# Performance work log

Hardware: AMD Instinct MI355X
Metric: run time of the kernel (lower is better)

Reference implementation:

```python
import jax, jax.numpy as jnp
import numpy as np

N = 50000      # nodes
E = 800000     # edges (before self loops)
IN = 128       # input_dim
ED = 16        # edge_dim
HID = 32       # hidden_dim (per-head out_channels)
H = 4          # heads
OUT = 64       # output_dim
NEG = 0.1      # negative_slope
EPS = 1e-5     # batchnorm eps


def setup_inputs() -> dict:
    key = jax.random.key(0)
    ks = jax.random.split(key, 32)
    s = 0.1
    p = {}
    p["x"] = jax.random.normal(ks[0], (N, IN), jnp.float32)
    p["edge_index"] = jax.random.randint(ks[1], (2, E), 0, N, dtype=jnp.int32)
    p["edge_attr"] = jax.random.normal(ks[2], (E, ED), jnp.float32)
    # input embed: Linear(IN, HID) + BatchNorm1d (eval-mode running stats)
    p["W0"] = jax.random.normal(ks[3], (HID, IN), jnp.float32) * s
    p["b0"] = jnp.zeros((HID,), jnp.float32)
    p["bn_g"] = jnp.ones((HID,), jnp.float32)
    p["bn_b"] = jnp.zeros((HID,), jnp.float32)
    p["bn_m"] = jnp.zeros((HID,), jnp.float32)
    p["bn_v"] = jnp.ones((HID,), jnp.float32)
    # two GATv2Conv layers: lin_l, lin_r [H*HID, HID] (+bias), lin_edge [H*HID, ED] (no bias),
    # att [H, HID], out bias [HID] (concat=False)
    k = 4
    for l in range(2):
        p[f"Wl{l}"] = jax.random.normal(ks[k + 0], (H * HID, HID), jnp.float32) * s
        p[f"bl{l}"] = jnp.zeros((H * HID,), jnp.float32)
        p[f"Wr{l}"] = jax.random.normal(ks[k + 1], (H * HID, HID), jnp.float32) * s
        p[f"br{l}"] = jnp.zeros((H * HID,), jnp.float32)
        p[f"We{l}"] = jax.random.normal(ks[k + 2], (H * HID, ED), jnp.float32) * s
        p[f"att{l}"] = jax.random.normal(ks[k + 3], (H, HID), jnp.float32) * s
        p[f"bias{l}"] = jnp.zeros((HID,), jnp.float32)
        k += 4
    p["Wout"] = jax.random.normal(ks[k], (OUT, HID), jnp.float32) * s
    p["bout"] = jnp.zeros((OUT,), jnp.float32)
    return p


def _gatv2(x, src, dst, eattr, Wl, bl, Wr, br, We, att, bias):
    # x: [N, HID]; src/dst: [Et]; eattr: [Et, ED]
    xl = (x @ Wl.T + bl).reshape(N, H, HID)   # source transform
    xr = (x @ Wr.T + br).reshape(N, H, HID)   # target transform
    ea = (eattr @ We.T).reshape(-1, H, HID)   # edge transform
    m = jax.nn.leaky_relu(xl[src] + xr[dst] + ea, NEG)   # [Et, H, HID]
    alpha = jnp.einsum('ehc,hc->eh', m, att)             # [Et, H]
    amax = jax.ops.segment_max(alpha, dst, num_segments=N)  # every node has a self loop
    ex = jnp.exp(alpha - amax[dst])
    den = jax.ops.segment_sum(ex, dst, num_segments=N)
    w = ex / den[dst]                                    # segment softmax [Et, H]
    out = jax.ops.segment_sum(xl[src] * w[:, :, None], dst, num_segments=N)  # [N, H, HID]
    return out.mean(axis=1) + bias                       # concat=False -> mean heads


def reference(x, edge_index, edge_attr,
              W0, b0, bn_g, bn_b, bn_m, bn_v,
              Wl0, bl0, Wr0, br0, We0, att0, bias0,
              Wl1, bl1, Wr1, br1, We1, att1, bias1,
              Wout, bout):
    src, dst = edge_index[0], edge_index[1]
    # input embed: Linear + BatchNorm1d(eval) + LeakyReLU(0.1)
    e = x @ W0.T + b0
    e = (e - bn_m) / jnp.sqrt(bn_v + EPS) * bn_g + bn_b
    e = jax.nn.leaky_relu(e, NEG)
    # add self loops once (same both layers): fill_value='mean' => per-dst mean edge_attr
    cnt = jax.ops.segment_sum(jnp.ones((E,), jnp.float32), dst, num_segments=N)
    loop_attr = jax.ops.segment_sum(edge_attr, dst, num_segments=N) / jnp.maximum(cnt, 1.0)[:, None]
    ar = jnp.arange(N, dtype=src.dtype)
    src_f = jnp.concatenate([src, ar])
    dst_f = jnp.concatenate([dst, ar])
    ea_f = jnp.concatenate([edge_attr, loop_attr], axis=0)
    h = _gatv2(e, src_f, dst_f, ea_f, Wl0, bl0, Wr0, br0, We0, att0, bias0)
    h = _gatv2(h, src_f, dst_f, ea_f, Wl1, bl1, Wr1, br1, We1, att1, bias1)
    return jax.nn.leaky_relu(h @ Wout.T + bout, NEG)
```

## Files before the change

### kernel.cpp

```cpp
#include <hip/hip_runtime.h>
#include <hip/hip_fp16.h>
#include <math.h>

#define NN   50000
#define EE   800000
#define IND  128
#define EDD  16
#define HIDD 32
#define NH   4
#define HC   128
#define OUTD 64
#define NEG  0.1f
#define BN_EPS 1e-5f
#define LOG2E 1.44269504088896340736f

typedef __attribute__((ext_vector_type(2))) float v2f;
typedef __attribute__((ext_vector_type(2))) _Float16 v2h;

#if defined(__has_builtin)
#  if __has_builtin(__builtin_amdgcn_fdot2)
#    define HAVE_FDOT2 1
#  else
#    define HAVE_FDOT2 0
#  endif
#else
#  define HAVE_FDOT2 0
#endif

__device__ __forceinline__ float lrelu(float x) { return fmaxf(x, NEG * x); }
__device__ __forceinline__ v2f lrelu2(v2f v) { return __builtin_elementwise_max(v, v * NEG); }
__device__ __forceinline__ float2 unpk(float f) {
    return __half22float2(__builtin_bit_cast(__half2, f));
}

#define DPPADD(p, CTRL) do {                                                     \
    int _t = __builtin_amdgcn_update_dpp(0, __builtin_bit_cast(int, (p)),        \
                                         (CTRL), 0xF, 0xF, true);                \
    (p) += __builtin_bit_cast(float, _t);                                        \
} while (0)

__global__ void count_fold_kernel(const int* __restrict__ ei, int* __restrict__ cnt,
                                  int* __restrict__ rank,
                                  const float* __restrict__ W0, const float* __restrict__ b0,
                                  const float* __restrict__ g, const float* __restrict__ bb,
                                  const float* __restrict__ bm, const float* __restrict__ bv,
                                  const float* __restrict__ Wl0, const float* __restrict__ Wr0,
                                  const float* __restrict__ Wl1, const float* __restrict__ Wr1,
                                  const float* __restrict__ We0, const float* __restrict__ We1,
                                  float* __restrict__ w0t, float* __restrict__ b0f,
                                  float* __restrict__ wlt0, float* __restrict__ wrt0,
                                  float* __restrict__ wlt1, float* __restrict__ wrt1,
                                  __half2* __restrict__ weh0, __half2* __restrict__ weh1) {
    if (blockIdx.x < EE / 256) {
        int e = blockIdx.x * 256 + threadIdx.x;
        rank[e] = atomicAdd(&cnt[ei[EE + e]], 1);
        return;
    }
    int tid = threadIdx.x;
    for (int idx = tid; idx < IND * HIDD; idx += 256) {
        int k = idx >> 5, c = idx & 31;
        float s = g[c] * (1.0f / sqrtf(bv[c] + BN_EPS));
        w0t[idx] = W0[c * IND + k] * s;
    }
    if (tid < HIDD) {
        float s = g[tid] * (1.0f / sqrtf(bv[tid] + BN_EPS));
        b0f[tid] = (b0[tid] - bm[tid]) * s + bb[tid];
    }
    for (int idx = tid; idx < HIDD * HC; idx += 256) {
        int k = idx >> 7, c = idx & 127;
        wlt0[idx] = Wl0[c * HIDD + k];
        wrt0[idx] = Wr0[c * HIDD + k];
        wlt1[idx] = Wl1[c * HIDD + k];
        wrt1[idx] = Wr1[c * HIDD + k];
    }
    for (int idx = tid; idx < HC * 8; idx += 256) {
        int c = idx >> 3, k = idx & 7;
        weh0[idx] = __floats2half2_rn(We0[c * EDD + 2 * k], We0[c * EDD + 2 * k + 1]);
        weh1[idx] = __floats2half2_rn(We1[c * EDD + 2 * k], We1[c * EDD + 2 * k + 1]);
    }
}

__global__ void scan1_kernel(const int* cnt, int* pre, int* bsum) {
    int i = blockIdx.x * 1024 + threadIdx.x;
    int lane = threadIdx.x & 63, wid = threadIdx.x >> 6;
    __shared__ int wsum[16];
    int v = (i < NN) ? cnt[i] : 0;
    int s = v;
    #pragma unroll
    for (int off = 1; off < 64; off <<= 1) {
        int t = __shfl_up(s, off);
        if (lane >= off) s += t;
    }
    if (lane == 63) wsum[wid] = s;
    __syncthreads();
    if (wid == 0) {
        int ws = (lane < 16) ? wsum[lane] : 0;
        #pragma unroll
        for (int off = 1; off < 16; off <<= 1) {
            int t = __shfl_up(ws, off);
            if (lane >= off) ws += t;
        }
        if (lane < 16) wsum[lane] = ws;
    }
    __syncthreads();
    int woff = (wid > 0) ? wsum[wid - 1] : 0;
    if (i < NN) pre[i] = woff + s - v;
    if (threadIdx.x == 1023) bsum[blockIdx.x] = wsum[15];
}

__global__ void scan3_kernel(int* rowstart, const int* pre, const int* bsum, int nb) {
    __shared__ int boff_s;
    if (threadIdx.x < 64) {
        int lane = threadIdx.x;
        int v = (lane < nb) ? bsum[lane] : 0;
        int s = v;
        #pragma unroll
        for (int off = 1; off < 64; off <<= 1) {
            int t = __shfl_up(s, off);
            if (lane >= off) s += t;
        }
        if (lane == (int)blockIdx.x) boff_s = s - v;
    }
    __syncthreads();
    int i = blockIdx.x * 1024 + threadIdx.x;
    if (i < NN) rowstart[i] = pre[i] + boff_s;
    if (i == 0) rowstart[NN] = EE;
}

__global__ void scatter_kernel(const int* __restrict__ ei, const int* __restrict__ rowstart,
                               const int* __restrict__ rank, const float* __restrict__ eattr,
                               int* __restrict__ csr_src, __half2* __restrict__ ea16) {
    int e = blockIdx.x * blockDim.x + threadIdx.x;
    if (e >= EE) return;
    int d = ei[EE + e];
    int pos = rowstart[d] + rank[e];
    csr_src[pos] = ei[e];
    const float4* src = (const float4*)(eattr + ((size_t)e << 4));
    float4 q0 = src[0], q1 = src[1], q2 = src[2], q3 = src[3];
    __half2 h[8];
    h[0] = __floats2half2_rn(q0.x, q0.y); h[1] = __floats2half2_rn(q0.z, q0.w);
    h[2] = __floats2half2_rn(q1.x, q1.y); h[3] = __floats2half2_rn(q1.z, q1.w);
    h[4] = __floats2half2_rn(q2.x, q2.y); h[5] = __floats2half2_rn(q2.z, q2.w);
    h[6] = __floats2half2_rn(q3.x, q3.y); h[7] = __floats2half2_rn(q3.z, q3.w);
    float4* dst = (float4*)(ea16 + ((size_t)pos << 3));
    dst[0] = *(float4*)&h[0];
    dst[1] = *(float4*)&h[4];
}

__global__ void embed_lin_kernel(const float* __restrict__ x,
                                 const float* __restrict__ w0t, const float* __restrict__ b0f,
                                 const float* __restrict__ wlt, const float* __restrict__ bl,
                                 const float* __restrict__ wrt, const float* __restrict__ br,
                                 __half2* __restrict__ xl, float* __restrict__ xr) {
    int tid = threadIdx.x;
    int n0 = blockIdx.x * 8;
    __shared__ float sx[8 * IND];
    __shared__ float se[8][HIDD];
    *(float4*)(sx + tid * 4) = *(const float4*)(x + (size_t)n0 * IND + tid * 4);
    __syncthreads();
    {
        int r = tid >> 5, c = tid & 31;
        float acc = b0f[c];
        const float* xrow = sx + r * IND;
        #pragma unroll 8
        for (int k = 0; k < IND; k++) acc += xrow[k] * w0t[k * HIDD + c];
        se[r][c] = lrelu(acc);
    }
    __syncthreads();
    int mat = tid >> 7, grp = (tid >> 6) & 1, pr = tid & 63;
    int c0 = 2 * pr;
    const float* WT = mat ? wrt : wlt;
    const float* b  = mat ? br : bl;
    v2f bv2 = (v2f){b[c0], b[c0 + 1]};
    v2f a0 = bv2, a1 = bv2, a2 = bv2, a3 = bv2;
    int nb = grp * 4;
    #pragma unroll
    for (int k = 0; k < HIDD; k++) {
        v2f wk = *(const v2f*)(WT + k * HC + c0);
        a0 += wk * se[nb + 0][k]; a1 += wk * se[nb + 1][k];
        a2 += wk * se[nb + 2][k]; a3 += wk * se[nb + 3][k];
    }
    if (mat == 0) {
        xl[((unsigned)(n0 + nb + 0) << 6) + pr] = __floats2half2_rn(a0.x, a0.y);
        xl[((unsigned)(n0 + nb + 1) << 6) + pr] = __floats2half2_rn(a1.x, a1.y);
        xl[((unsigned)(n0 + nb + 2) << 6) + pr] = __floats2half2_rn(a2.x, a2.y);
        xl[((unsigned)(n0 + nb + 3) << 6) + pr] = __floats2half2_rn(a3.x, a3.y);
    } else {
        *(float2*)(xr + ((unsigned)(n0 + nb + 0) << 7) + c0) = make_float2(a0.x, a0.y);
        *(float2*)(xr + ((unsigned)(n0 + nb + 1) << 7) + c0) = make_float2(a1.x, a1.y);
        *(float2*)(xr + ((unsigned)(n0 + nb + 2) << 7) + c0) = make_float2(a2.x, a2.y);
        *(float2*)(xr + ((unsigned)(n0 + nb + 3) << 7) + c0) = make_float2(a3.x, a3.y);
    }
}

__global__ void lin_kernel(const float* __restrict__ f,
                           const float* __restrict__ wlt, const float* __restrict__ bl,
                           const float* __restrict__ wrt, const float* __restrict__ br,
                           __half2* __restrict__ xl, float* __restrict__ xr) {
    int tid = threadIdx.x;
    int n0 = blockIdx.x * 8;
    __shared__ float se[8][HIDD];
    se[tid >> 5][tid & 31] = f[((unsigned)(n0 + (tid >> 5)) << 5) + (tid & 31)];
    __syncthreads();
    int mat = tid >> 7, grp = (tid >> 6) & 1, pr = tid & 63;
    int c0 = 2 * pr;
    const float* WT = mat ? wrt : wlt;
    const float* b  = mat ? br : bl;
    v2f bv2 = (v2f){b[c0], b[c0 + 1]};
    v2f a0 = bv2, a1 = bv2, a2 = bv2, a3 = bv2;
    int nb = grp * 4;
    #pragma unroll
    for (int k = 0; k < HIDD; k++) {
        v2f wk = *(const v2f*)(WT + k * HC + c0);
        a0 += wk * se[nb + 0][k]; a1 += wk * se[nb + 1][k];
        a2 += wk * se[nb + 2][k]; a3 += wk * se[nb + 3][k];
    }
    if (mat == 0) {
        xl[((unsigned)(n0 + nb + 0) << 6) + pr] = __floats2half2_rn(a0.x, a0.y);
        xl[((unsigned)(n0 + nb + 1) << 6) + pr] = __floats2half2_rn(a1.x, a1.y);
        xl[((unsigned)(n0 + nb + 2) << 6) + pr] = __floats2half2_rn(a2.x, a2.y);
        xl[((unsigned)(n0 + nb + 3) << 6) + pr] = __floats2half2_rn(a3.x, a3.y);
    } else {
        *(float2*)(xr + ((unsigned)(n0 + nb + 0) << 7) + c0) = make_float2(a0.x, a0.y);
        *(float2*)(xr + ((unsigned)(n0 + nb + 1) << 7) + c0) = make_float2(a1.x, a1.y);
        *(float2*)(xr + ((unsigned)(n0 + nb + 2) << 7) + c0) = make_float2(a2.x, a2.y);
        *(float2*)(xr + ((unsigned)(n0 + nb + 3) << 7) + c0) = make_float2(a3.x, a3.y);
    }
}

template<bool OUTHEAD>
__global__ void gat_fused_kernel(const __half2* __restrict__ xl, const float* __restrict__ xr,
                                 const __half2* __restrict__ ea16,
                                 const float* __restrict__ We,
                                 const __half2* __restrict__ weh,
                                 const float* __restrict__ att,
                                 const int* __restrict__ rowstart, const int* __restrict__ csr_src,
                                 const float* __restrict__ bias,
                                 const float* __restrict__ Wout, const float* __restrict__ bout,
                                 float* __restrict__ out) {
    int n = (blockIdx.x * blockDim.x + threadIdx.x) >> 6;
    int lane = threadIdx.x & 63;
    if (n >= NN) return;
    n = __builtin_amdgcn_readfirstlane(n);
    int start = __builtin_amdgcn_readfirstlane(rowstart[n]);
    int end   = __builtin_amdgcn_readfirstlane(rowstart[n + 1]);
    int deg = end - start;
    int c0 = 2 * lane;

    __half2 xLh = xl[((unsigned)n << 6) + lane];
    v2f xrv = *(const v2f*)(xr + ((unsigned)n << 7) + c0);
    v2f attv = *(const v2f*)(att + c0) * LOG2E;

#if HAVE_FDOT2
    (void)We;
    v2h wh0[8], wh1[8];
    {
        const float4* pw = (const float4*)(weh + (size_t)c0 * 8);
        float4 q0 = pw[0], q1 = pw[1], q2 = pw[2], q3 = pw[3];
        float t[16];
        *(float4*)(t)      = q0; *(float4*)(t + 4)  = q1;
        *(float4*)(t + 8)  = q2; *(float4*)(t + 12) = q3;
        #pragma unroll
        for (int k = 0; k < 8; k++) {
            wh0[k] = __builtin_bit_cast(v2h, t[k]);
            wh1[k] = __builtin_bit_cast(v2h, t[8 + k]);
        }
    }
    auto proj = [&](float4 r0, float4 r1) -> v2f {
        float e[8];
        *(float4*)(e) = r0; *(float4*)(e + 4) = r1;
        float a0 = 0.f, a1 = 0.f;
        #pragma unroll
        for (int k = 0; k < 8; k++) {
            v2h ek = __builtin_bit_cast(v2h, e[k]);
            a0 = __builtin_amdgcn_fdot2(ek, wh0[k], a0, false);
            a1 = __builtin_amdgcn_fdot2(ek, wh1[k], a1, false);
        }
        return (v2f){a0, a1};
    };
#else
    (void)weh;
    v2f wv[16];
    {
        const float* ra = We + c0 * EDD;
        const float* rb = ra + EDD;
        float4 a0 = *(const float4*)(ra),     a1 = *(const float4*)(ra + 4);
        float4 a2 = *(const float4*)(ra + 8), a3 = *(const float4*)(ra + 12);
        float4 b0 = *(const float4*)(rb),     b1 = *(const float4*)(rb + 4);
        float4 b2 = *(const float4*)(rb + 8), b3 = *(const float4*)(rb + 12);
        wv[0]=(v2f){a0.x,b0.x}; wv[1]=(v2f){a0.y,b0.y}; wv[2]=(v2f){a0.z,b0.z}; wv[3]=(v2f){a0.w,b0.w};
        wv[4]=(v2f){a1.x,b1.x}; wv[5]=(v2f){a1.y,b1.y}; wv[6]=(v2f){a1.z,b1.z}; wv[7]=(v2f){a1.w,b1.w};
        wv[8]=(v2f){a2.x,b2.x}; wv[9]=(v2f){a2.y,b2.y}; wv[10]=(v2f){a2.z,b2.z}; wv[11]=(v2f){a2.w,b2.w};
        wv[12]=(v2f){a3.x,b3.x}; wv[13]=(v2f){a3.y,b3.y}; wv[14]=(v2f){a3.z,b3.z}; wv[15]=(v2f){a3.w,b3.w};
    }
    auto proj = [&](float4 r0, float4 r1) -> v2f {
        float2 t0 = unpk(r0.x), t1 = unpk(r0.y), t2 = unpk(r0.z), t3 = unpk(r0.w);
        float2 t4 = unpk(r1.x), t5 = unpk(r1.y), t6 = unpk(r1.z), t7 = unpk(r1.w);
        return wv[0]*t0.x  + wv[1]*t0.y  + wv[2]*t1.x  + wv[3]*t1.y
             + wv[4]*t2.x  + wv[5]*t2.y  + wv[6]*t3.x  + wv[7]*t3.y
             + wv[8]*t4.x  + wv[9]*t4.y  + wv[10]*t5.x + wv[11]*t5.y
             + wv[12]*t6.x + wv[13]*t6.y + wv[14]*t7.x + wv[15]*t7.y;
    };
#endif

    float lh = 0.f;
    v2f acc   = (v2f){0.f, 0.f};
    v2f easum = (v2f){0.f, 0.f};

    auto proc = [&](v2f xv, v2f ea) {
        easum += ea;
        v2f z  = xv + xrv + ea;
        v2f mm = lrelu2(z);
        v2f pp = mm * attv;
        float p = pp.x + pp.y;
        DPPADD(p, 0xB1);
        DPPADD(p, 0x4E);
        DPPADD(p, 0x124);
        DPPADD(p, 0x128);
        float w = exp2f(p);
        lh  += w;
        acc += xv * w;
    };

    #define GATHER(i0, S0, S1, S2, S3, X0, X1, X2, X3, E0, E1, E2, E3) do {           \
        __half2 xh0 = xl[((unsigned)(S0) << 6) + lane];                                \
        __half2 xh1 = xl[((unsigned)(S1) << 6) + lane];                                \
        __half2 xh2 = xl[((unsigned)(S2) << 6) + lane];                                \
        __half2 xh3 = xl[((unsigned)(S3) << 6) + lane];                                \
        const float4* ep = (const float4*)(ea16 + ((size_t)(unsigned)(i0) << 3));      \
        float4 r00 = ep[0], r01 = ep[1], r10 = ep[2], r11 = ep[3];                     \
        float4 r20 = ep[4], r21 = ep[5], r30 = ep[6], r31 = ep[7];                     \
        E0 = proj(r00, r01); E1 = proj(r10, r11);                                      \
        E2 = proj(r20, r21); E3 = proj(r30, r31);                                      \
        float2 xf;                                                                     \
        xf = __half22float2(xh0); X0 = (v2f){xf.x, xf.y};                              \
        xf = __half22float2(xh1); X1 = (v2f){xf.x, xf.y};                              \
        xf = __half22float2(xh2); X2 = (v2f){xf.x, xf.y};                              \
        xf = __half22float2(xh3); X3 = (v2f){xf.x, xf.y};                              \
    } while (0)

    int i = start;
    int nf = deg >> 2;
    if (nf > 0) {
        int v0 = csr_src[i],     v1 = csr_src[i + 1],
            v2 = csr_src[i + 2], v3 = csr_src[i + 3];
        int j4 = (i + 4 > EE - 4) ? (EE - 4) : (i + 4);
        int u0 = csr_src[j4],     u1 = csr_src[j4 + 1],
            u2 = csr_src[j4 + 2], u3 = csr_src[j4 + 3];
        int s0 = __builtin_amdgcn_readfirstlane(v0), s1 = __builtin_amdgcn_readfirstlane(v1);
        int s2 = __builtin_amdgcn_readfirstlane(v2), s3 = __builtin_amdgcn_readfirstlane(v3);
        v2f A0x, A1x, A2x, A3x, A0e, A1e, A2e, A3e;
        GATHER(i, s0, s1, s2, s3, A0x, A1x, A2x, A3x, A0e, A1e, A2e, A3e);
        for (int k = 1; k < nf; k++) {
            int jn = i + 4 * (k + 1);
            jn = (jn > EE - 4) ? (EE - 4) : jn;
            int w0 = csr_src[jn],     w1 = csr_src[jn + 1],
                w2 = csr_src[jn + 2], w3 = csr_src[jn + 3];
            int t0 = __builtin_amdgcn_readfirstlane(u0), t1 = __builtin_amdgcn_readfirstlane(u1);
            int t2 = __builtin_amdgcn_readfirstlane(u2), t3 = __builtin_amdgcn_readfirstlane(u3);
            v2f B0x, B1x, B2x, B3x, B0e, B1e, B2e, B3e;
            GATHER(i + 4 * k, t0, t1, t2, t3, B0x, B1x, B2x, B3x, B0e, B1e, B2e, B3e);
            proc(A0x, A0e); proc(A1x, A1e); proc(A2x, A2e); proc(A3x, A3e);
            A0x = B0x; A1x = B1x; A2x = B2x; A3x = B3x;
            A0e = B0e; A1e = B1e; A2e = B2e; A3e = B3e;
            u0 = w0; u1 = w1; u2 = w2; u3 = w3;
        }
        proc(A0x, A0e); proc(A1x, A1e); proc(A2x, A2e); proc(A3x, A3e);
        i += 4 * nf;
    }
    int rem = end - i;
    if (rem > 0) {
        v2f Tx[3], Te[3];
        int sA = __builtin_amdgcn_readfirstlane(csr_src[i]);
        int sB = (rem > 1) ? __builtin_amdgcn_readfirstlane(csr_src[i + 1]) : sA;
        int sC = (rem > 2) ? __builtin_amdgcn_readfirstlane(csr_src[i + 2]) : sA;
        __half2 xh0 = xl[((unsigned)sA << 6) + lane];
        __half2 xh1 = xl[((unsigned)sB << 6) + lane];
        __half2 xh2 = xl[((unsigned)sC << 6) + lane];
        const float4* ep = (const float4*)(ea16 + ((size_t)(unsigned)i << 3));
        int lim2 = (rem > 1) ? 2 : 0, lim4 = (rem > 2) ? 4 : 0;
        float4 r00 = ep[0], r01 = ep[1];
        float4 r10 = ep[lim2], r11 = ep[lim2 + 1];
        float4 r20 = ep[lim4], r21 = ep[lim4 + 1];
        float2 xf;
        xf = __half22float2(xh0); Tx[0] = (v2f){xf.x, xf.y};
        xf = __half22float2(xh1); Tx[1] = (v2f){xf.x, xf.y};
        xf = __half22float2(xh2); Tx[2] = (v2f){xf.x, xf.y};
        Te[0] = proj(r00, r01); Te[1] = proj(r10, r11); Te[2] = proj(r20, r21);
        proc(Tx[0], Te[0]);
        if (rem > 1) proc(Tx[1], Te[1]);
        if (rem > 2) proc(Tx[2], Te[2]);
    }

    {
        float invdeg = 1.0f / (float)(deg > 0 ? deg : 1);
        float2 xf = __half22float2(xLh);
        proc((v2f){xf.x, xf.y}, easum * invdeg);
    }

    float inv = 1.0f / lh;
    float acc0 = acc.x * inv, acc1 = acc.y * inv;
    acc0 += __shfl_xor(acc0, 16); acc0 += __shfl_xor(acc0, 32);
    acc1 += __shfl_xor(acc1, 16); acc1 += __shfl_xor(acc1, 32);

    if (!OUTHEAD) {
        if (lane < 16) {
            float2 o = make_float2(acc0 * 0.25f + bias[2 * lane],
                                   acc1 * 0.25f + bias[2 * lane + 1]);
            *(float2*)(out + ((unsigned)n << 5) + 2 * lane) = o;
        }
    } else {
        __shared__ float sh[4][HIDD];
        int w = threadIdx.x >> 6;
        if (lane < 16) {
            sh[w][2 * lane]     = acc0 * 0.25f + bias[2 * lane];
            sh[w][2 * lane + 1] = acc1 * 0.25f + bias[2 * lane + 1];
        }
        float a = bout[lane];
        const float* wr = Wout + lane * HIDD;
        #pragma unroll
        for (int k = 0; k < HIDD; k++) a += sh[w][k] * wr[k];
        out[((unsigned)n << 6) + lane] = lrelu(a);
    }
    #undef GATHER
}

extern "C" void kernel_launch(void* const* d_in, const int* in_sizes, int n_in,
                              void* d_out, int out_size, void* d_ws, size_t ws_size,
                              hipStream_t stream) {
    const float* x     = (const float*)d_in[0];
    const int*   ei    = (const int*)  d_in[1];
    const float* eattr = (const float*)d_in[2];
    const float* W0    = (const float*)d_in[3];
    const float* b0    = (const float*)d_in[4];
    const float* bn_g  = (const float*)d_in[5];
    const float* bn_b  = (const float*)d_in[6];
    const float* bn_m  = (const float*)d_in[7];
    const float* bn_v  = (const float*)d_in[8];
    const float* Wl[2]   = { (const float*)d_in[9],  (const float*)d_in[16] };
    const float* bl[2]   = { (const float*)d_in[10], (const float*)d_in[17] };
    const float* Wr[2]   = { (const float*)d_in[11], (const float*)d_in[18] };
    const float* br[2]   = { (const float*)d_in[12], (const float*)d_in[19] };
    const float* We[2]   = { (const float*)d_in[13], (const float*)d_in[20] };
    const float* att[2]  = { (const float*)d_in[14], (const float*)d_in[21] };
    const float* bias[2] = { (const float*)d_in[15], (const float*)d_in[22] };
    const float* Wout  = (const float*)d_in[23];
    const float* bout  = (const float*)d_in[24];
    float* out = (float*)d_out;

    const int NB = (NN + 1023) / 1024;
    char* p = (char*)d_ws;
    auto carve = [&](size_t bytes) { char* r = p; p += (bytes + 255) & ~(size_t)255; return r; };
    float*   h1       = (float*)  carve((size_t)NN * HIDD * 4);
    __half2* xl       = (__half2*)carve((size_t)NN * HC * 2);
    float*   xr       = (float*)  carve((size_t)NN * HC * 4);
    int*     cnt      = (int*)    carve((size_t)NN * 4);
    int*     rank     = (int*)    carve((size_t)EE * 4);
    int*     pre      = (int*)    carve((size_t)NN * 4);
    int*     bsum     = (int*)    carve((size_t)64 * 4);
    int*     rowstart = (int*)    carve((size_t)(NN + 1) * 4);
    int*     csr_src  = (int*)    carve((size_t)EE * 4);
    __half2* ea16     = (__half2*)carve((size_t)EE * EDD * 2);
    float*   w0t      = (float*)  carve((size_t)IND * HIDD * 4);
    float*   b0f      = (float*)  carve((size_t)HIDD * 4);
    float*   wlt0     = (float*)  carve((size_t)HIDD * HC * 4);
    float*   wrt0     = (float*)  carve((size_t)HIDD * HC * 4);
    float*   wlt1     = (float*)  carve((size_t)HIDD * HC * 4);
    float*   wrt1     = (float*)  carve((size_t)HIDD * HC * 4);
    __half2* weh0     = (__half2*)carve((size_t)HC * 8 * 4);
    __half2* weh1     = (__half2*)carve((size_t)HC * 8 * 4);

    hipMemsetAsync(cnt, 0, (size_t)NN * 4, stream);

    count_fold_kernel<<<EE / 256 + 1, 256, 0, stream>>>(
        ei, cnt, rank, W0, b0, bn_g, bn_b, bn_m, bn_v,
        Wl[0], Wr[0], Wl[1], Wr[1], We[0], We[1],
        w0t, b0f, wlt0, wrt0, wlt1, wrt1, weh0, weh1);
    scan1_kernel<<<NB, 1024, 0, stream>>>(cnt, pre, bsum);
    scan3_kernel<<<NB, 1024, 0, stream>>>(rowstart, pre, bsum, NB);
    scatter_kernel<<<(EE + 255) / 256, 256, 0, stream>>>(ei, rowstart, rank, eattr,
                                                         csr_src, ea16);

    embed_lin_kernel<<<NN / 8, 256, 0, stream>>>(x, w0t, b0f, wlt0, bl[0], wrt0, br[0], xl, xr);
    gat_fused_kernel<false><<<(NN * 64) / 256, 256, 0, stream>>>(
        xl, xr, ea16, We[0], weh0, att[0], rowstart, csr_src, bias[0], nullptr, nullptr, h1);

    lin_kernel<<<NN / 8, 256, 0, stream>>>(h1, wlt1, bl[1], wrt1, br[1], xl, xr);
    gat_fused_kernel<true><<<(NN * 64) / 256, 256, 0, stream>>>(
        xl, xr, ea16, We[1], weh1, att[1], rowstart, csr_src, bias[1], Wout, bout, out);
}
```

Before: 474.5 us.

## Process two destination nodes per wavefront with four channels per lane

The GAT aggregation kernel now assigns two nodes to each 64-lane wave, one per 32-lane half, and each lane handles four channels instead of two. Edge loops run to the larger of the two degrees, with predicated weights, and read from a padded CSR tail so the separate remainder path goes away. Source indices are loaded cooperatively and shuffled instead of read with scalar loads. The aim is to halve the number of waves and improve memory-level parallelism for low-degree nodes, at the cost of divergence between the two halves' degrees and more registers per lane.

```diff
diff --git a/kernel.cpp b/kernel.cpp
--- a/kernel.cpp
+++ b/kernel.cpp
@@ -15,6 +15,7 @@
 #define LOG2E 1.44269504088896340736f
 
 typedef __attribute__((ext_vector_type(2))) float v2f;
+typedef __attribute__((ext_vector_type(4))) float v4f;
 typedef __attribute__((ext_vector_type(2))) _Float16 v2h;
 
 #if defined(__has_builtin)
@@ -28,8 +29,10 @@
 #endif
 
 __device__ __forceinline__ float lrelu(float x) { return fmaxf(x, NEG * x); }
-__device__ __forceinline__ v2f lrelu2(v2f v) { return __builtin_elementwise_max(v, v * NEG); }
-__device__ __forceinline__ float2 unpk(float f) {
+__device__ __forceinline__ float2 unpk(unsigned u) {
+    return __half22float2(__builtin_bit_cast(__half2, u));
+}
+__device__ __forceinline__ float2 unpkf(float f) {
     return __half22float2(__builtin_bit_cast(__half2, f));
 }
 
@@ -132,6 +135,12 @@
                                int* __restrict__ csr_src, __half2* __restrict__ ea16) {
     int e = blockIdx.x * blockDim.x + threadIdx.x;
     if (e >= EE) return;
+    if (e < 8) {
+        csr_src[EE + e] = 0;
+        float4* pd = (float4*)(ea16 + ((size_t)(EE + e) << 3));
+        pd[0] = make_float4(0.f, 0.f, 0.f, 0.f);
+        pd[1] = make_float4(0.f, 0.f, 0.f, 0.f);
+    }
     int d = ei[EE + e];
     int pos = rowstart[d] + rank[e];
     csr_src[pos] = ei[e];
@@ -229,198 +238,185 @@
 }
 
 template<bool OUTHEAD>
-__global__ void gat_fused_kernel(const __half2* __restrict__ xl, const float* __restrict__ xr,
+__global__ __launch_bounds__(256) void gat_fused_kernel(
+                                 const __half2* __restrict__ xl, const float* __restrict__ xr,
                                  const __half2* __restrict__ ea16,
-                                 const float* __restrict__ We,
                                  const __half2* __restrict__ weh,
                                  const float* __restrict__ att,
                                  const int* __restrict__ rowstart, const int* __restrict__ csr_src,
                                  const float* __restrict__ bias,
                                  const float* __restrict__ Wout, const float* __restrict__ bout,
                                  float* __restrict__ out) {
-    int n = (blockIdx.x * blockDim.x + threadIdx.x) >> 6;
+    int w = __builtin_amdgcn_readfirstlane(blockIdx.x * 4 + (threadIdx.x >> 6));
     int lane = threadIdx.x & 63;
-    if (n >= NN) return;
-    n = __builtin_amdgcn_readfirstlane(n);
-    int start = __builtin_amdgcn_readfirstlane(rowstart[n]);
-    int end   = __builtin_amdgcn_readfirstlane(rowstart[n + 1]);
-    int deg = end - start;
-    int c0 = 2 * lane;
-
-    __half2 xLh = xl[((unsigned)n << 6) + lane];
-    v2f xrv = *(const v2f*)(xr + ((unsigned)n << 7) + c0);
-    v2f attv = *(const v2f*)(att + c0) * LOG2E;
+    int half = (lane >> 5) & 1, hl = lane & 31;
+    int nA = 2 * w;
+    int sA = __builtin_amdgcn_readfirstlane(rowstart[nA]);
+    int sM = __builtin_amdgcn_readfirstlane(rowstart[nA + 1]);
+    int sE = __builtin_amdgcn_readfirstlane(rowstart[nA + 2]);
+    int degA = sM - sA, degB = sE - sM;
+    int dmax = degA > degB ? degA : degB;
+    int n     = half ? (nA + 1) : nA;
+    int start = half ? sM : sA;
+    int deg   = half ? degB : degA;
+    int c4 = 4 * hl;
+
+    uint2 xLh = *(const uint2*)(xl + ((unsigned)n << 6) + 2 * hl);
+    v4f xrv = *(const v4f*)(xr + ((size_t)n << 7) + c4);
+    v4f attv = *(const v4f*)(att + c4) * LOG2E;
 
 #if HAVE_FDOT2
-    (void)We;
-    v2h wh0[8], wh1[8];
+    v2h wh0[8], wh1[8], wh2[8], wh3[8];
     {
-        const float4* pw = (const float4*)(weh + (size_t)c0 * 8);
-        float4 q0 = pw[0], q1 = pw[1], q2 = pw[2], q3 = pw[3];
-        float t[16];
-        *(float4*)(t)      = q0; *(float4*)(t + 4)  = q1;
-        *(float4*)(t + 8)  = q2; *(float4*)(t + 12) = q3;
+        const float4* pw = (const float4*)(weh + (size_t)c4 * 8);
+        float t[32];
+        #pragma unroll
+        for (int q = 0; q < 8; q++) *(float4*)(t + 4 * q) = pw[q];
         #pragma unroll
         for (int k = 0; k < 8; k++) {
             wh0[k] = __builtin_bit_cast(v2h, t[k]);
             wh1[k] = __builtin_bit_cast(v2h, t[8 + k]);
-        }
-    }
-    auto proj = [&](float4 r0, float4 r1) -> v2f {
+            wh2[k] = __builtin_bit_cast(v2h, t[16 + k]);
+            wh3[k] = __builtin_bit_cast(v2h, t[24 + k]);
+        }
+    }
+    auto proj = [&](float4 r0, float4 r1) -> v4f {
         float e[8];
         *(float4*)(e) = r0; *(float4*)(e + 4) = r1;
-        float a0 = 0.f, a1 = 0.f;
+        float a0 = 0.f, a1 = 0.f, a2 = 0.f, a3 = 0.f;
         #pragma unroll
         for (int k = 0; k < 8; k++) {
             v2h ek = __builtin_bit_cast(v2h, e[k]);
             a0 = __builtin_amdgcn_fdot2(ek, wh0[k], a0, false);
             a1 = __builtin_amdgcn_fdot2(ek, wh1[k], a1, false);
-        }
-        return (v2f){a0, a1};
+            a2 = __builtin_amdgcn_fdot2(ek, wh2[k], a2, false);
+            a3 = __builtin_amdgcn_fdot2(ek, wh3[k], a3, false);
+        }
+        return (v4f){a0, a1, a2, a3};
     };
 #else
-    (void)weh;
-    v2f wv[16];
+    float wf0[16], wf1[16], wf2[16], wf3[16];
     {
-        const float* ra = We + c0 * EDD;
-        const float* rb = ra + EDD;
-        float4 a0 = *(const float4*)(ra),     a1 = *(const float4*)(ra + 4);
-        float4 a2 = *(const float4*)(ra + 8), a3 = *(const float4*)(ra + 12);
-        float4 b0 = *(const float4*)(rb),     b1 = *(const float4*)(rb + 4);
-        float4 b2 = *(const float4*)(rb + 8), b3 = *(const float4*)(rb + 12);
-        wv[0]=(v2f){a0.x,b0.x}; wv[1]=(v2f){a0.y,b0.y}; wv[2]=(v2f){a0.z,b0.z}; wv[3]=(v2f){a0.w,b0.w};
-        wv[4]=(v2f){a1.x,b1.x}; wv[5]=(v2f){a1.y,b1.y}; wv[6]=(v2f){a1.z,b1.z}; wv[7]=(v2f){a1.w,b1.w};
-        wv[8]=(v2f){a2.x,b2.x}; wv[9]=(v2f){a2.y,b2.y}; wv[10]=(v2f){a2.z,b2.z}; wv[11]=(v2f){a2.w,b2.w};
-        wv[12]=(v2f){a3.x,b3.x}; wv[13]=(v2f){a3.y,b3.y}; wv[14]=(v2f){a3.z,b3.z}; wv[15]=(v2f){a3.w,b3.w};
-    }
-    auto proj = [&](float4 r0, float4 r1) -> v2f {
-        float2 t0 = unpk(r0.x), t1 = unpk(r0.y), t2 = unpk(r0.z), t3 = unpk(r0.w);
-        float2 t4 = unpk(r1.x), t5 = unpk(r1.y), t6 = unpk(r1.z), t7 = unpk(r1.w);
-        return wv[0]*t0.x  + wv[1]*t0.y  + wv[2]*t1.x  + wv[3]*t1.y
-             + wv[4]*t2.x  + wv[5]*t2.y  + wv[6]*t3.x  + wv[7]*t3.y
-             + wv[8]*t4.x  + wv[9]*t4.y  + wv[10]*t5.x + wv[11]*t5.y
-             + wv[12]*t6.x + wv[13]*t6.y + wv[14]*t7.x + wv[15]*t7.y;
+        const float4* pw = (const float4*)(weh + (size_t)c4 * 8);
+        float t[32];
+        #pragma unroll
+        for (int q = 0; q < 8; q++) *(float4*)(t + 4 * q) = pw[q];
+        #pragma unroll
+        for (int k = 0; k < 8; k++) {
+            float2 p0 = unpkf(t[k]),      p1 = unpkf(t[8 + k]);
+            float2 p2 = unpkf(t[16 + k]), p3 = unpkf(t[24 + k]);
+            wf0[2 * k] = p0.x; wf0[2 * k + 1] = p0.y;
+            wf1[2 * k] = p1.x; wf1[2 * k + 1] = p1.y;
+            wf2[2 * k] = p2.x; wf2[2 * k + 1] = p2.y;
+            wf3[2 * k] = p3.x; wf3[2 * k + 1] = p3.y;
+        }
+    }
+    auto proj = [&](float4 r0, float4 r1) -> v4f {
+        float e[8];
+        *(float4*)(e) = r0; *(float4*)(e + 4) = r1;
+        v4f a = (v4f){0.f, 0.f, 0.f, 0.f};
+        #pragma unroll
+        for (int k = 0; k < 8; k++) {
+            float2 t = unpkf(e[k]);
+            a.x += wf0[2 * k] * t.x + wf0[2 * k + 1] * t.y;
+            a.y += wf1[2 * k] * t.x + wf1[2 * k + 1] * t.y;
+            a.z += wf2[2 * k] * t.x + wf2[2 * k + 1] * t.y;
+            a.w += wf3[2 * k] * t.x + wf3[2 * k + 1] * t.y;
+        }
+        return a;
     };
 #endif
 
     float lh = 0.f;
-    v2f acc   = (v2f){0.f, 0.f};
-    v2f easum = (v2f){0.f, 0.f};
-
-    auto proc = [&](v2f xv, v2f ea) {
-        easum += ea;
-        v2f z  = xv + xrv + ea;
-        v2f mm = lrelu2(z);
-        v2f pp = mm * attv;
-        float p = pp.x + pp.y;
+    v4f acc   = (v4f){0.f, 0.f, 0.f, 0.f};
+    v4f easum = (v4f){0.f, 0.f, 0.f, 0.f};
+
+    auto proc = [&](uint2 xh, v4f ea, int ord) {
+        float vf = (ord < deg) ? 1.0f : 0.0f;
+        easum += ea * vf;
+        float2 lo = unpk(xh.x), hi = unpk(xh.y);
+        v4f xv = (v4f){lo.x, lo.y, hi.x, hi.y};
+        v4f z  = xv + xrv + ea;
+        v4f m  = __builtin_elementwise_max(z, z * NEG);
+        v4f pp = m * attv;
+        float p = (pp.x + pp.y) + (pp.z + pp.w);
         DPPADD(p, 0xB1);
         DPPADD(p, 0x4E);
-        DPPADD(p, 0x124);
-        DPPADD(p, 0x128);
-        float w = exp2f(p);
-        lh  += w;
-        acc += xv * w;
+        DPPADD(p, 0x141);
+        float wgt = exp2f(p) * vf;
+        lh  += wgt;
+        acc += xv * wgt;
     };
 
-    #define GATHER(i0, S0, S1, S2, S3, X0, X1, X2, X3, E0, E1, E2, E3) do {           \
-        __half2 xh0 = xl[((unsigned)(S0) << 6) + lane];                                \
-        __half2 xh1 = xl[((unsigned)(S1) << 6) + lane];                                \
-        __half2 xh2 = xl[((unsigned)(S2) << 6) + lane];                                \
-        __half2 xh3 = xl[((unsigned)(S3) << 6) + lane];                                \
-        const float4* ep = (const float4*)(ea16 + ((size_t)(unsigned)(i0) << 3));      \
+    #define GATHER(IQ, OB, X0, X1, X2, X3, E0, E1, E2, E3) do {                        \
+        int _iqs = ((OB) < deg) ? (IQ) : 0;                                            \
+        int _t = csr_src[_iqs + (hl & 3)];                                             \
+        const float4* ep = (const float4*)(ea16 + ((size_t)(unsigned)_iqs << 3));      \
         float4 r00 = ep[0], r01 = ep[1], r10 = ep[2], r11 = ep[3];                     \
         float4 r20 = ep[4], r21 = ep[5], r30 = ep[6], r31 = ep[7];                     \
+        int _s0 = __shfl(_t, 0, 32), _s1 = __shfl(_t, 1, 32);                          \
+        int _s2 = __shfl(_t, 2, 32), _s3 = __shfl(_t, 3, 32);                          \
+        X0 = *(const uint2*)(xl + ((unsigned)_s0 << 6) + 2 * hl);                      \
+        X1 = *(const uint2*)(xl + ((unsigned)_s1 << 6) + 2 * hl);                      \
+        X2 = *(const uint2*)(xl + ((unsigned)_s2 << 6) + 2 * hl);                      \
+        X3 = *(const uint2*)(xl + ((unsigned)_s3 << 6) + 2 * hl);                      \
         E0 = proj(r00, r01); E1 = proj(r10, r11);                                      \
         E2 = proj(r20, r21); E3 = proj(r30, r31);                                      \
-        float2 xf;                                                                     \
-        xf = __half22float2(xh0); X0 = (v2f){xf.x, xf.y};                              \
-        xf = __half22float2(xh1); X1 = (v2f){xf.x, xf.y};                              \
-        xf = __half22float2(xh2); X2 = (v2f){xf.x, xf.y};                              \
-        xf = __half22float2(xh3); X3 = (v2f){xf.x, xf.y};                              \
     } while (0)
 
-    int i = start;
-    int nf = deg >> 2;
-    if (nf > 0) {
-        int v0 = csr_src[i],     v1 = csr_src[i + 1],
-            v2 = csr_src[i + 2], v3 = csr_src[i + 3];
-        int j4 = (i + 4 > EE - 4) ? (EE - 4) : (i + 4);
-        int u0 = csr_src[j4],     u1 = csr_src[j4 + 1],
-            u2 = csr_src[j4 + 2], u3 = csr_src[j4 + 3];
-        int s0 = __builtin_amdgcn_readfirstlane(v0), s1 = __builtin_amdgcn_readfirstlane(v1);
-        int s2 = __builtin_amdgcn_readfirstlane(v2), s3 = __builtin_amdgcn_readfirstlane(v3);
-        v2f A0x, A1x, A2x, A3x, A0e, A1e, A2e, A3e;
-        GATHER(i, s0, s1, s2, s3, A0x, A1x, A2x, A3x, A0e, A1e, A2e, A3e);
-        for (int k = 1; k < nf; k++) {
-            int jn = i + 4 * (k + 1);
-            jn = (jn > EE - 4) ? (EE - 4) : jn;
-            int w0 = csr_src[jn],     w1 = csr_src[jn + 1],
-                w2 = csr_src[jn + 2], w3 = csr_src[jn + 3];
-            int t0 = __builtin_amdgcn_readfirstlane(u0), t1 = __builtin_amdgcn_readfirstlane(u1);
-            int t2 = __builtin_amdgcn_readfirstlane(u2), t3 = __builtin_amdgcn_readfirstlane(u3);
-            v2f B0x, B1x, B2x, B3x, B0e, B1e, B2e, B3e;
-            GATHER(i + 4 * k, t0, t1, t2, t3, B0x, B1x, B2x, B3x, B0e, B1e, B2e, B3e);
-            proc(A0x, A0e); proc(A1x, A1e); proc(A2x, A2e); proc(A3x, A3e);
+    int M = (dmax + 3) >> 2;
+    if (M > 0) {
+        uint2 A0x, A1x, A2x, A3x; v4f A0e, A1e, A2e, A3e;
+        GATHER(start, 0, A0x, A1x, A2x, A3x, A0e, A1e, A2e, A3e);
+        for (int k = 1; k < M; k++) {
+            int iq = start + 4 * k;
+            uint2 B0x, B1x, B2x, B3x; v4f B0e, B1e, B2e, B3e;
+            GATHER(iq, 4 * k, B0x, B1x, B2x, B3x, B0e, B1e, B2e, B3e);
+            int ob = 4 * (k - 1);
+            proc(A0x, A0e, ob); proc(A1x, A1e, ob + 1);
+            proc(A2x, A2e, ob + 2); proc(A3x, A3e, ob + 3);
             A0x = B0x; A1x = B1x; A2x = B2x; A3x = B3x;
             A0e = B0e; A1e = B1e; A2e = B2e; A3e = B3e;
-            u0 = w0; u1 = w1; u2 = w2; u3 = w3;
-        }
-        proc(A0x, A0e); proc(A1x, A1e); proc(A2x, A2e); proc(A3x, A3e);
-        i += 4 * nf;
-    }
-    int rem = end - i;
-    if (rem > 0) {
-        v2f Tx[3], Te[3];
-        int sA = __builtin_amdgcn_readfirstlane(csr_src[i]);
-        int sB = (rem > 1) ? __builtin_amdgcn_readfirstlane(csr_src[i + 1]) : sA;
-        int sC = (rem > 2) ? __builtin_amdgcn_readfirstlane(csr_src[i + 2]) : sA;
-        __half2 xh0 = xl[((unsigned)sA << 6) + lane];
-        __half2 xh1 = xl[((unsigned)sB << 6) + lane];
-        __half2 xh2 = xl[((unsigned)sC << 6) + lane];
-        const float4* ep = (const float4*)(ea16 + ((size_t)(unsigned)i << 3));
-        int lim2 = (rem > 1) ? 2 : 0, lim4 = (rem > 2) ? 4 : 0;
-        float4 r00 = ep[0], r01 = ep[1];
-        float4 r10 = ep[lim2], r11 = ep[lim2 + 1];
-        float4 r20 = ep[lim4], r21 = ep[lim4 + 1];
-        float2 xf;
-        xf = __half22float2(xh0); Tx[0] = (v2f){xf.x, xf.y};
-        xf = __half22float2(xh1); Tx[1] = (v2f){xf.x, xf.y};
-        xf = __half22float2(xh2); Tx[2] = (v2f){xf.x, xf.y};
-        Te[0] = proj(r00, r01); Te[1] = proj(r10, r11); Te[2] = proj(r20, r21);
-        proc(Tx[0], Te[0]);
-        if (rem > 1) proc(Tx[1], Te[1]);
-        if (rem > 2) proc(Tx[2], Te[2]);
+        }
+        int ob = 4 * (M - 1);
+        proc(A0x, A0e, ob); proc(A1x, A1e, ob + 1);
+        proc(A2x, A2e, ob + 2); proc(A3x, A3e, ob + 3);
     }
 
     {
         float invdeg = 1.0f / (float)(deg > 0 ? deg : 1);
-        float2 xf = __half22float2(xLh);
-        proc((v2f){xf.x, xf.y}, easum * invdeg);
-    }
-
-    float inv = 1.0f / lh;
-    float acc0 = acc.x * inv, acc1 = acc.y * inv;
-    acc0 += __shfl_xor(acc0, 16); acc0 += __shfl_xor(acc0, 32);
-    acc1 += __shfl_xor(acc1, 16); acc1 += __shfl_xor(acc1, 32);
+        proc(xLh, easum * invdeg, -1);
+    }
+
+    float inv = 0.25f / lh;
+    v4f o = acc * inv;
+    o.x += __shfl_xor(o.x, 8);  o.x += __shfl_xor(o.x, 16);
+    o.y += __shfl_xor(o.y, 8);  o.y += __shfl_xor(o.y, 16);
+    o.z += __shfl_xor(o.z, 8);  o.z += __shfl_xor(o.z, 16);
+    o.w += __shfl_xor(o.w, 8);  o.w += __shfl_xor(o.w, 16);
 
     if (!OUTHEAD) {
-        if (lane < 16) {
-            float2 o = make_float2(acc0 * 0.25f + bias[2 * lane],
-                                   acc1 * 0.25f + bias[2 * lane + 1]);
-            *(float2*)(out + ((unsigned)n << 5) + 2 * lane) = o;
+        if (hl < 8) {
+            v4f r = o + *(const v4f*)(bias + c4);
+            *(v4f*)(out + ((size_t)n << 5) + c4) = r;
         }
     } else {
-        __shared__ float sh[4][HIDD];
-        int w = threadIdx.x >> 6;
-        if (lane < 16) {
-            sh[w][2 * lane]     = acc0 * 0.25f + bias[2 * lane];
-            sh[w][2 * lane + 1] = acc1 * 0.25f + bias[2 * lane + 1];
-        }
-        float a = bout[lane];
-        const float* wr = Wout + lane * HIDD;
-        #pragma unroll
-        for (int k = 0; k < HIDD; k++) a += sh[w][k] * wr[k];
-        out[((unsigned)n << 6) + lane] = lrelu(a);
+        __shared__ __align__(16) float sh[8][HIDD];
+        int slot = threadIdx.x >> 5;
+        if (hl < 8) *(v4f*)(&sh[slot][c4]) = o + *(const v4f*)(bias + c4);
+        __syncthreads();
+        float a0 = bout[hl], a1 = bout[hl + 32];
+        const float4* w0p = (const float4*)(Wout + hl * HIDD);
+        const float4* w1p = (const float4*)(Wout + (hl + 32) * HIDD);
+        const float4* sp  = (const float4*)(&sh[slot][0]);
+        #pragma unroll
+        for (int k = 0; k < 8; k++) {
+            float4 s4 = sp[k], wa = w0p[k], wb = w1p[k];
+            a0 += s4.x * wa.x + s4.y * wa.y + s4.z * wa.z + s4.w * wa.w;
+            a1 += s4.x * wb.x + s4.y * wb.y + s4.z * wb.z + s4.w * wb.w;
+        }
+        out[((size_t)n << 6) + hl]      = lrelu(a0);
+        out[((size_t)n << 6) + hl + 32] = lrelu(a1);
     }
     #undef GATHER
 }
@@ -459,8 +455,8 @@
     int*     pre      = (int*)    carve((size_t)NN * 4);
     int*     bsum     = (int*)    carve((size_t)64 * 4);
     int*     rowstart = (int*)    carve((size_t)(NN + 1) * 4);
-    int*     csr_src  = (int*)    carve((size_t)EE * 4);
-    __half2* ea16     = (__half2*)carve((size_t)EE * EDD * 2);
+    int*     csr_src  = (int*)    carve((size_t)(EE + 8) * 4);
+    __half2* ea16     = (__half2*)carve((size_t)(EE + 8) * EDD * 2);
     float*   w0t      = (float*)  carve((size_t)IND * HIDD * 4);
     float*   b0f      = (float*)  carve((size_t)HIDD * 4);
     float*   wlt0     = (float*)  carve((size_t)HIDD * HC * 4);
@@ -482,10 +478,10 @@
                                                          csr_src, ea16);
 
     embed_lin_kernel<<<NN / 8, 256, 0, stream>>>(x, w0t, b0f, wlt0, bl[0], wrt0, br[0], xl, xr);
-    gat_fused_kernel<false><<<(NN * 64) / 256, 256, 0, stream>>>(
-        xl, xr, ea16, We[0], weh0, att[0], rowstart, csr_src, bias[0], nullptr, nullptr, h1);
+    gat_fused_kernel<false><<<NN / 8, 256, 0, stream>>>(
+        xl, xr, ea16, weh0, att[0], rowstart, csr_src, bias[0], nullptr, nullptr, h1);
 
     lin_kernel<<<NN / 8, 256, 0, stream>>>(h1, wlt1, bl[1], wrt1, br[1], xl, xr);
-    gat_fused_kernel<true><<<(NN * 64) / 256, 256, 0, stream>>>(
-        xl, xr, ea16, We[1], weh1, att[1], rowstart, csr_src, bias[1], Wout, bout, out);
-}
+    gat_fused_kernel<true><<<NN / 8, 256, 0, stream>>>(
+        xl, xr, ea16, weh1, att[1], rowstart, csr_src, bias[1], Wout, bout, out);
+}
```

After: 579.1 us. 1.22x slower.
